# Performance work log

Measured on AMD Instinct MI355X. Metric: run time of the kernel, lower is better.

## Reference

```python
import jax, jax.numpy as jnp
import numpy as np

N, H, OUT, R, E, B = 50000, 64, 64, 50, 800000, 4  # nodes, hidden, out, relations, edges, blocks


def _glorot(k, shape):
    fan_in, fan_out = shape[-2], shape[-1]
    s = (6.0 / (fan_in + fan_out)) ** 0.5
    return jax.random.uniform(k, shape, jnp.float32, -s, s)


def setup_inputs() -> dict:
    key = jax.random.key(0)
    ks = jax.random.split(key, 12)
    db = H // B
    inp = {
        "x": jax.random.normal(ks[0], (N, H), jnp.float32),
        "edge_index": jax.random.randint(ks[1], (2, E), 0, N),
        "edge_type": jax.random.randint(ks[2], (E,), 0, R),
        # hidden RGCNConv layers: block-diagonal relation weights [R,B,db,db]
        "w0_rel": _glorot(ks[3], (R, B, db, db)),
        "w0_root": _glorot(ks[4], (H, H)),
        "b0": jnp.zeros((H,), jnp.float32),
        "w1_rel": _glorot(ks[5], (R, B, db, db)),
        "w1_root": _glorot(ks[6], (H, H)),
        "b1": jnp.zeros((H,), jnp.float32),
        # final RGCNConv: full per-relation weights [R,H,OUT]
        "w2_rel": _glorot(ks[7], (R, H, OUT)),
        "w2_root": _glorot(ks[8], (H, OUT)),
        "b2": jnp.zeros((OUT,), jnp.float32),
    }
    return inp


def _rgcn_layer(x, src, dst, etype, w_rel, w_root, bias):
    """RGCNConv: per-relation mean aggregation of neighbor features, relation-typed
    transform, plus root (self) transform and bias. Instead of gathering a per-edge
    weight (huge), we segment-sum neighbor features per (dst node, relation) and do
    one batched matmul over relations -- same math, far less traffic."""
    n, d = x.shape
    seg = dst * R + etype                                   # combined (node,rel) id
    msgs = x[src]                                           # [E, d] gather
    s = jax.ops.segment_sum(msgs, seg, num_segments=n * R).reshape(n, R, d)
    cnt = jax.ops.segment_sum(jnp.ones((msgs.shape[0],), x.dtype), seg,
                              num_segments=n * R).reshape(n, R, 1)
    s = s / jnp.maximum(cnt, 1.0)                           # mean per relation
    if w_rel.ndim == 4:                                     # block-diagonal decomposition
        nb, db, do = w_rel.shape[1], w_rel.shape[2], w_rel.shape[3]
        agg = jnp.einsum('nrbd,rbde->nbe', s.reshape(n, R, nb, db), w_rel)
        agg = agg.reshape(n, nb * do)
    else:                                                   # full per-relation weight
        agg = jnp.einsum('nrd,rde->ne', s, w_rel)
    return agg + x @ w_root + bias


def reference(x, edge_index, edge_type,
              w0_rel, w0_root, b0,
              w1_rel, w1_root, b1,
              w2_rel, w2_root, b2):
    src, dst = edge_index[0], edge_index[1]
    h = jax.nn.relu(_rgcn_layer(x, src, dst, edge_type, w0_rel, w0_root, b0))
    # dropout: eval mode (identity)
    h = jax.nn.relu(_rgcn_layer(h, src, dst, edge_type, w1_rel, w1_root, b1))
    return _rgcn_layer(h, src, dst, edge_type, w2_rel, w2_root, b2)
```

## Files before the change

### kernel.cpp

```cpp
#include <hip/hip_runtime.h>
#include <cstdint>
#include <cstddef>

#define N_NODES 50000
#define HDIM 64
#define NREL 50
#define NEDGE 800000
#define DCHUNK 196
#define CHUNKSH 11
#define NCHUNK 25
#define NKEYS (NCHUNK * NREL)
#define KCH 5
#define CAP 36864
#define TILE 8192

typedef __attribute__((ext_vector_type(8))) short short8;
typedef __attribute__((ext_vector_type(4))) float f32x4;

static __device__ __forceinline__ unsigned short f2bf(float f) {
  union { float f; unsigned int u; } v; v.f = f;
  unsigned int u = v.u;
  unsigned int r = (u + 0x7FFFu + ((u >> 16) & 1u)) >> 16;
  return (unsigned short)r;
}


__global__ __launch_bounds__(256) void csort_k(const int* __restrict__ ei,
                                               const int* __restrict__ et,
                                               int* __restrict__ ccur,
                                               int2* __restrict__ ce) {
  __shared__ int chist[32];
  __shared__ int cbase[32];
  int tid = threadIdx.x;
  if (tid < 32) chist[tid] = 0;
  __syncthreads();
  int ebase = blockIdx.x * 1280 + tid;
  int src_[5], dr_[5], ch_[5], loc_[5];
#pragma unroll
  for (int i = 0; i < 5; ++i) {
    int e = ebase + i * 256;
    int src = ei[e];
    int dst = ei[NEDGE + e];
    int r = et[e];
    int ch = dst >> CHUNKSH;
    src_[i] = src;
    dr_[i] = (dst << 6) | r;
    ch_[i] = ch;
    loc_[i] = atomicAdd(&chist[ch], 1);
  }
  __syncthreads();
  if (tid < NCHUNK && chist[tid] > 0)
    cbase[tid] = atomicAdd(&ccur[tid], chist[tid]);
  __syncthreads();
#pragma unroll
  for (int i = 0; i < 5; ++i)
    ce[(size_t)ch_[i] * CAP + cbase[ch_[i]] + loc_[i]] = make_int2(src_[i], dr_[i]);
}

__global__ __launch_bounds__(1024) void msplit_k(const int2* __restrict__ ce,
                                                 const int* __restrict__ ccur,
                                                 int* __restrict__ dcur,
                                                 int* __restrict__ kcur,
                                                 int* __restrict__ dkr) {
  __shared__ int dhist[2048], dbase[2048];
  __shared__ int rhist[64], rbase[64];
  int c = blockIdx.y;
  int len = ccur[c];
  int t0 = blockIdx.x * TILE;
  if (t0 >= len) return;
  int tid = threadIdx.x;
  dhist[tid] = 0;
  dhist[tid + 1024] = 0;
  if (tid < 64) rhist[tid] = 0;
  __syncthreads();
  int n = min(TILE, len - t0);
  const int2* seg = ce + (size_t)c * CAP + t0;
  int pk[8], dr_[8];
#pragma unroll
  for (int k = 0; k < 8; ++k) {
    int j = tid + k * 1024;
    if (j < n) {
      int2 v = seg[j];
      dr_[k] = v.y;
      int d11 = (v.y >> 6) & 2047;
      int rel = v.y & 63;
      int dl = atomicAdd(&dhist[d11], 1);
      int rl = atomicAdd(&rhist[rel], 1);
      pk[k] = (dl << 16) | rl;
    } else {
      pk[k] = -1;
    }
  }
  __syncthreads();
  int h0 = dhist[tid];
  if (h0 > 0) dbase[tid] = atomicAdd(&dcur[(c << CHUNKSH) + tid], h0);
  int h1 = dhist[tid + 1024];
  if (h1 > 0) dbase[tid + 1024] = atomicAdd(&dcur[(c << CHUNKSH) + tid + 1024], h1);
  if (tid < NREL) {
    int hr = rhist[tid];
    if (hr > 0) rbase[tid] = atomicAdd(&kcur[c * NREL + tid], hr);
  }
  __syncthreads();
#pragma unroll
  for (int k = 0; k < 8; ++k) {
    if (pk[k] >= 0) {
      int d11 = (dr_[k] >> 6) & 2047;
      int rel = dr_[k] & 63;
      int drank = dbase[d11] + (pk[k] >> 16);
      int krank = rbase[rel] + (pk[k] & 0xFFFF);
      dkr[(size_t)c * CAP + t0 + tid + k * 1024] = (drank << 16) | krank;
    }
  }
}

__global__ __launch_bounds__(256) void kscan_k(const int* __restrict__ kcur,
                                               int* __restrict__ key_off) {
  __shared__ int a[256], bb[256];
  int t = threadIdx.x;
  int base = t * KCH;
  int local[KCH];
  int s = 0;
#pragma unroll
  for (int i = 0; i < KCH; ++i) {
    int k = base + i;
    int v = (k < NKEYS) ? kcur[k] : 0;
    local[i] = s;
    s += v;
  }
  a[t] = s;
  __syncthreads();
  bool flip = false;
  for (int off = 1; off < 256; off <<= 1) {
    int* c = flip ? bb : a;
    int* n = flip ? a : bb;
    int x = c[t];
    if (t >= off) x += c[t - off];
    n[t] = x;
    __syncthreads();
    flip = !flip;
  }
  int incl = (flip ? bb : a)[t];
  int excl = incl - s;
#pragma unroll
  for (int i = 0; i < KCH; ++i) {
    int k = base + i;
    if (k < NKEYS) key_off[k] = excl + local[i];
  }
  if (t == 255) key_off[NKEYS] = incl;
}

__global__ __launch_bounds__(256) void dsA_k(const int* __restrict__ dcnt,
                                             int* __restrict__ psum) {
  __shared__ int red[256];
  int t = threadIdx.x, b = blockIdx.x;
  int idx = b * DCHUNK + t;
  int v = (t < DCHUNK && idx < N_NODES) ? dcnt[idx] : 0;
  red[t] = v;
  __syncthreads();
  for (int s = 128; s > 0; s >>= 1) {
    if (t < s) red[t] += red[t + s];
    __syncthreads();
  }
  if (t == 0) psum[b] = red[0];
}

__global__ __launch_bounds__(256) void dsB_k(const int* __restrict__ psum,
                                             int* __restrict__ psb,
                                             int* __restrict__ dst_off) {
  __shared__ int a[256], bb[256];
  int t = threadIdx.x;
  int v = psum[t];
  a[t] = v;
  __syncthreads();
  bool flip = false;
  for (int off = 1; off < 256; off <<= 1) {
    int* c = flip ? bb : a;
    int* n = flip ? a : bb;
    int x = c[t];
    if (t >= off) x += c[t - off];
    n[t] = x;
    __syncthreads();
    flip = !flip;
  }
  int incl = (flip ? bb : a)[t];
  psb[t] = incl - v;
  if (t == 255) dst_off[N_NODES] = incl;
}

__global__ __launch_bounds__(256) void dsC_k(const int* __restrict__ dcnt,
                                             const int* __restrict__ psb,
                                             int* __restrict__ dst_off) {
  __shared__ int a[256], bb[256];
  int t = threadIdx.x, b = blockIdx.x;
  int idx = b * DCHUNK + t;
  int v = (t < DCHUNK && idx < N_NODES) ? dcnt[idx] : 0;
  a[t] = v;
  __syncthreads();
  bool flip = false;
  for (int off = 1; off < 256; off <<= 1) {
    int* c = flip ? bb : a;
    int* n = flip ? a : bb;
    int x = c[t];
    if (t >= off) x += c[t - off];
    n[t] = x;
    __syncthreads();
    flip = !flip;
  }
  int incl = (flip ? bb : a)[t];
  if (t < DCHUNK && idx < N_NODES) dst_off[idx] = psb[b] + (incl - v);
}

__global__ __launch_bounds__(1024) void place_k(const int2* __restrict__ ce,
                                                const int* __restrict__ ccur,
                                                const int* __restrict__ dkr,
                                                const int* __restrict__ key_off,
                                                const int* __restrict__ dst_off,
                                                int* __restrict__ es,
                                                int* __restrict__ rpr) {
  int c = blockIdx.y;
  int len = ccur[c];
  int t0 = blockIdx.x * TILE;
  if (t0 >= len) return;
  int tid = threadIdx.x;
  int n = min(TILE, len - t0);
  size_t base = (size_t)c * CAP + t0;
#pragma unroll
  for (int k = 0; k < 8; ++k) {
    int j = tid + k * 1024;
    if (j < n) {
      int2 v = ce[base + j];
      int dk = dkr[base + j];
      int dst = v.y >> 6;
      int rel = v.y & 63;
      int key = c * NREL + rel;
      int pos = key_off[key] + (dk & 0xFFFF);
      int dp = dst_off[dst] + (dk >> 16);
      es[pos] = v.x;
      rpr[dp] = (pos << 6) | rel;
    }
  }
}

__global__ __launch_bounds__(256) void coef_k(const int* __restrict__ rpr,
                                              const int* __restrict__ dst_off,
                                              float* __restrict__ coefd) {
  int lane = threadIdx.x & 63;
  int wv = (blockIdx.x * 256 + threadIdx.x) >> 6;
  int half = lane >> 5, l = lane & 31;
  int dst = wv * 2 + half;
  if (dst >= N_NODES) return;
  int lo = dst_off[dst], hi = dst_off[dst + 1];
  for (int j = lo + l; j < hi; j += 32) {
    int r = rpr[j] & 63;
    int c = 0;
    for (int k = lo; k < hi; ++k) c += ((rpr[k] & 63) == r);
    coefd[j] = 1.0f / (float)c;
  }
}

__global__ void prep_k(const float* __restrict__ w0, const float* __restrict__ w1,
                       const float* __restrict__ w2,
                       const float* __restrict__ wr0f, const float* __restrict__ wr1f,
                       const float* __restrict__ wr2f,
                       unsigned short* __restrict__ Wt0, unsigned short* __restrict__ Wt1,
                       unsigned short* __restrict__ Wt2,
                       unsigned short* __restrict__ Wr0, unsigned short* __restrict__ Wr1,
                       unsigned short* __restrict__ Wr2) {
  int idx = blockIdx.x * 256 + threadIdx.x;
  if (idx < NREL * 4096) {
    int r = idx >> 12, rem = idx & 4095, d = rem >> 6, o = rem & 63;
    int tpos = (r << 12) + (o << 6) + d;
    Wt2[tpos] = f2bf(w2[idx]);
    int b = o >> 4;
    float v0 = 0.f, v1 = 0.f;
    if (b == (d >> 4)) {
      int widx = ((r * 4 + b) * 16 + (d & 15)) * 16 + (o & 15);
      v0 = w0[widx];
      v1 = w1[widx];
    }
    Wt0[tpos] = f2bf(v0);
    Wt1[tpos] = f2bf(v1);
  }
  if (idx < 4096) {
    int d = idx >> 6, o = idx & 63;
    int tpos = (o << 6) + d;
    Wr0[tpos] = f2bf(wr0f[idx]);
    Wr1[tpos] = f2bf(wr1f[idx]);
    Wr2[tpos] = f2bf(wr2f[idx]);
  }
}

__global__ void conv_k(const float* __restrict__ in, unsigned short* __restrict__ out) {
  int i = blockIdx.x * 256 + threadIdx.x;
  out[i] = f2bf(in[i]);
}


__global__ __launch_bounds__(256) void root_k(const unsigned short* __restrict__ xbf,
                                              const unsigned short* __restrict__ wr,
                                              const float* __restrict__ bias,
                                              unsigned short* __restrict__ hbf) {
  int wid = threadIdx.x >> 6, lane = threadIdx.x & 63;
  int n15 = lane & 15, quad = lane >> 4;
  int t = blockIdx.x * 4 + wid;
  if (t >= N_NODES / 16) return;
  short8 bfr[4][2];
#pragma unroll
  for (int nb = 0; nb < 4; ++nb)
#pragma unroll
    for (int k = 0; k < 2; ++k)
      bfr[nb][k] = *reinterpret_cast<const short8*>(wr + ((nb * 16 + n15) << 6) + k * 32 + quad * 8);
  float bv[4];
#pragma unroll
  for (int nb = 0; nb < 4; ++nb) bv[nb] = bias[nb * 16 + n15];

  int base = t * 16;
  const short8* xr = reinterpret_cast<const short8*>(xbf + (size_t)(base + n15) * 64);
  short8 a0 = xr[quad], a1 = xr[4 + quad];
  f32x4 acc[4];
#pragma unroll
  for (int nb = 0; nb < 4; ++nb) acc[nb] = (f32x4){0.f, 0.f, 0.f, 0.f};
#pragma unroll
  for (int nb = 0; nb < 4; ++nb) {
    acc[nb] = __builtin_amdgcn_mfma_f32_16x16x32_bf16(a0, bfr[nb][0], acc[nb], 0, 0, 0);
    acc[nb] = __builtin_amdgcn_mfma_f32_16x16x32_bf16(a1, bfr[nb][1], acc[nb], 0, 0, 0);
  }
#pragma unroll
  for (int i = 0; i < 4; ++i) {
    int node = base + quad * 4 + i;
#pragma unroll
    for (int nb = 0; nb < 4; ++nb)
      hbf[(size_t)node * 64 + nb * 16 + n15] = f2bf(acc[nb][i] + bv[nb]);
  }
}

__global__ __launch_bounds__(256) void edge_k(const unsigned short* __restrict__ xbf,
                                              const unsigned short* __restrict__ wt,
                                              const int* __restrict__ es,
                                              const int* __restrict__ key_off,
                                              unsigned short* __restrict__ msg) {
  int key = blockIdx.y;
  int lo = key_off[key], hi = key_off[key + 1];
  if (lo >= hi) return;
  int wid = threadIdx.x >> 6, lane = threadIdx.x & 63;
  int n15 = lane & 15, quad = lane >> 4;
  const unsigned short* wr = wt + ((size_t)(key % NREL) << 12);
  short8 bfr[4][2];
#pragma unroll
  for (int nb = 0; nb < 4; ++nb)
#pragma unroll
    for (int k = 0; k < 2; ++k)
      bfr[nb][k] = *reinterpret_cast<const short8*>(wr + ((nb * 16 + n15) << 6) + k * 32 + quad * 8);

  int ntiles = (hi - lo + 15) >> 4;
  for (int t = blockIdx.x * 4 + wid; t < ntiles; t += gridDim.x * 4) {
    int base = lo + t * 16;
    int eidx = base + n15;
    if (eidx > NEDGE - 1) eidx = NEDGE - 1;
    int src = es[eidx];
    const short8* xr = reinterpret_cast<const short8*>(xbf + (size_t)src * 64);
    short8 a0 = xr[quad], a1 = xr[4 + quad];
    f32x4 acc[4];
#pragma unroll
    for (int nb = 0; nb < 4; ++nb) acc[nb] = (f32x4){0.f, 0.f, 0.f, 0.f};
#pragma unroll
    for (int nb = 0; nb < 4; ++nb) {
      acc[nb] = __builtin_amdgcn_mfma_f32_16x16x32_bf16(a0, bfr[nb][0], acc[nb], 0, 0, 0);
      acc[nb] = __builtin_amdgcn_mfma_f32_16x16x32_bf16(a1, bfr[nb][1], acc[nb], 0, 0, 0);
    }
#pragma unroll
    for (int i = 0; i < 4; ++i) {
      int e2 = base + quad * 4 + i;
      if (e2 < hi) {
        size_t row = (size_t)e2 * 64;
#pragma unroll
        for (int nb = 0; nb < 4; ++nb)
          msg[row + nb * 16 + n15] = f2bf(acc[nb][i]);
      }
    }
  }
}

__global__ __launch_bounds__(256) void agg_k(const unsigned short* __restrict__ hbf,
                                             const unsigned short* __restrict__ msg,
                                             const float* __restrict__ coefd,
                                             const int* __restrict__ rpr,
                                             const int* __restrict__ dst_off,
                                             float* __restrict__ outf,
                                             unsigned short* __restrict__ outbf,
                                             int mode) {
  int lane = threadIdx.x & 63;
  int wv = (blockIdx.x * 256 + threadIdx.x) >> 6;
  int half = lane >> 5, l = lane & 31;
  int dst = wv * 2 + half;
  if (dst >= N_NODES) return;
  int lo = dst_off[dst], hi = dst_off[dst + 1];
  const unsigned int* h32 = reinterpret_cast<const unsigned int*>(hbf);
  unsigned int hu = __builtin_nontemporal_load(h32 + (size_t)dst * 32 + l);
  union { unsigned int u; float f; } hx, hy;
  hx.u = (hu & 0xFFFFu) << 16;
  hy.u = hu & 0xFFFF0000u;
  float ax = hx.f, ay = hy.f;
  const unsigned int* m32 = reinterpret_cast<const unsigned int*>(msg);
  int j = lo;
  for (; j + 4 <= hi; j += 4) {
    int q0 = rpr[j] >> 6, q1 = rpr[j + 1] >> 6, q2 = rpr[j + 2] >> 6, q3 = rpr[j + 3] >> 6;
    float c0 = coefd[j], c1 = coefd[j + 1], c2 = coefd[j + 2], c3 = coefd[j + 3];
    unsigned int u0 = __builtin_nontemporal_load(m32 + q0 * 32 + l);
    unsigned int u1 = __builtin_nontemporal_load(m32 + q1 * 32 + l);
    unsigned int u2 = __builtin_nontemporal_load(m32 + q2 * 32 + l);
    unsigned int u3 = __builtin_nontemporal_load(m32 + q3 * 32 + l);
    union { unsigned int u; float f; } cx, cy;
    cx.u = (u0 & 0xFFFFu) << 16; cy.u = u0 & 0xFFFF0000u; ax += c0 * cx.f; ay += c0 * cy.f;
    cx.u = (u1 & 0xFFFFu) << 16; cy.u = u1 & 0xFFFF0000u; ax += c1 * cx.f; ay += c1 * cy.f;
    cx.u = (u2 & 0xFFFFu) << 16; cy.u = u2 & 0xFFFF0000u; ax += c2 * cx.f; ay += c2 * cy.f;
    cx.u = (u3 & 0xFFFFu) << 16; cy.u = u3 & 0xFFFF0000u; ax += c3 * cx.f; ay += c3 * cy.f;
  }
  for (; j < hi; ++j) {
    float c = coefd[j];
    int pos = rpr[j] >> 6;
    unsigned int u = __builtin_nontemporal_load(m32 + pos * 32 + l);
    union { unsigned int u; float f; } cx, cy;
    cx.u = (u & 0xFFFFu) << 16;
    cy.u = u & 0xFFFF0000u;
    ax += c * cx.f;
    ay += c * cy.f;
  }
  if (mode == 0) {
    float fx = fmaxf(ax, 0.f), fy = fmaxf(ay, 0.f);
    unsigned int pk = ((unsigned int)f2bf(fy) << 16) | (unsigned int)f2bf(fx);
    *reinterpret_cast<unsigned int*>(outbf + (size_t)dst * 64 + 2 * l) = pk;
  } else {
    float2 o2; o2.x = ax; o2.y = ay;
    *reinterpret_cast<float2*>(outf + (size_t)dst * 64 + 2 * l) = o2;
  }
}


extern "C" void kernel_launch(void* const* d_in, const int* in_sizes, int n_in,
                              void* d_out, int out_size, void* d_ws, size_t ws_size,
                              hipStream_t stream) {
  const float* x   = (const float*)d_in[0];
  const int*   ei  = (const int*)d_in[1];
  const int*   et  = (const int*)d_in[2];
  const float* w0  = (const float*)d_in[3];
  const float* wr0 = (const float*)d_in[4];
  const float* b0  = (const float*)d_in[5];
  const float* w1  = (const float*)d_in[6];
  const float* wr1 = (const float*)d_in[7];
  const float* b1  = (const float*)d_in[8];
  const float* w2  = (const float*)d_in[9];
  const float* wr2 = (const float*)d_in[10];
  const float* b2  = (const float*)d_in[11];
  float* out = (float*)d_out;

  char* p = (char*)d_ws;
  auto take = [&](size_t bytes) -> char* {
    char* q = p;
    p += (bytes + 255) & ~(size_t)255;
    return q;
  };
  char*  zbase   = p;
  int*   ccur    = (int*)take(32 * 4);
  int*   dcur    = (int*)take((size_t)NCHUNK * 2048 * 4);
  int*   kcur    = (int*)take((size_t)NKEYS * 4);
  size_t zbytes  = (size_t)(p - zbase);
  int*   key_off = (int*)take((size_t)(NKEYS + 1) * 4);
  int*   dst_off = (int*)take((size_t)(N_NODES + 1) * 4);
  int*   psum    = (int*)take(256 * 4);
  int*   psb     = (int*)take(256 * 4);
  int2*  ce      = (int2*)take((size_t)NCHUNK * CAP * 8);
  int*   dkr     = (int*)take((size_t)NCHUNK * CAP * 4);
  int*   es      = (int*)take((size_t)NEDGE * 4);
  int*   rpr     = (int*)take((size_t)NEDGE * 4);
  float* coefd   = (float*)take((size_t)NEDGE * 4);
  unsigned short* xbf = (unsigned short*)take((size_t)N_NODES * 64 * 2);
  unsigned short* hbf = (unsigned short*)take((size_t)N_NODES * 64 * 2);
  unsigned short* msg = (unsigned short*)take((size_t)NEDGE * 64 * 2);
  unsigned short* Wt0 = (unsigned short*)take((size_t)NREL * 4096 * 2);
  unsigned short* Wt1 = (unsigned short*)take((size_t)NREL * 4096 * 2);
  unsigned short* Wt2 = (unsigned short*)take((size_t)NREL * 4096 * 2);
  unsigned short* Wr0 = (unsigned short*)take(4096 * 2);
  unsigned short* Wr1 = (unsigned short*)take(4096 * 2);
  unsigned short* Wr2 = (unsigned short*)take(4096 * 2);

  hipMemsetAsync(zbase, 0, zbytes, stream);
  csort_k<<<NEDGE / 1280, 256, 0, stream>>>(ei, et, ccur, ce);
  dim3 mg(5, NCHUNK);
  msplit_k<<<mg, 1024, 0, stream>>>(ce, ccur, dcur, kcur, dkr);
  kscan_k<<<1, 256, 0, stream>>>(kcur, key_off);
  dsA_k<<<256, 256, 0, stream>>>(dcur, psum);
  dsB_k<<<1, 256, 0, stream>>>(psum, psb, dst_off);
  dsC_k<<<256, 256, 0, stream>>>(dcur, psb, dst_off);
  place_k<<<mg, 1024, 0, stream>>>(ce, ccur, dkr, key_off, dst_off, es, rpr);
  coef_k<<<N_NODES / 8, 256, 0, stream>>>(rpr, dst_off, coefd);
  prep_k<<<(NREL * 4096 + 255) / 256, 256, 0, stream>>>(w0, w1, w2, wr0, wr1, wr2,
                                                        Wt0, Wt1, Wt2, Wr0, Wr1, Wr2);

  const int conv_blocks = N_NODES * 64 / 256;
  const int root_blocks = (N_NODES / 16 + 3) / 4;
  const int agg_blocks  = N_NODES / 8;
  dim3 eg(2, NKEYS);

  conv_k<<<conv_blocks, 256, 0, stream>>>(x, xbf);
  root_k<<<root_blocks, 256, 0, stream>>>(xbf, Wr0, b0, hbf);
  edge_k<<<eg, 256, 0, stream>>>(xbf, Wt0, es, key_off, msg);
  agg_k<<<agg_blocks, 256, 0, stream>>>(hbf, msg, coefd, rpr, dst_off, nullptr, xbf, 0);
  root_k<<<root_blocks, 256, 0, stream>>>(xbf, Wr1, b1, hbf);
  edge_k<<<eg, 256, 0, stream>>>(xbf, Wt1, es, key_off, msg);
  agg_k<<<agg_blocks, 256, 0, stream>>>(hbf, msg, coefd, rpr, dst_off, nullptr, xbf, 0);
  root_k<<<root_blocks, 256, 0, stream>>>(xbf, Wr2, b2, hbf);
  edge_k<<<eg, 256, 0, stream>>>(xbf, Wt2, es, key_off, msg);
  agg_k<<<agg_blocks, 256, 0, stream>>>(hbf, msg, coefd, rpr, dst_off, out, nullptr, 1);
}
```

Measured before the change: 379.4 us.

## Sub-bucket edges by source range within each relation key for gather locality

The per-(chunk, relation) edge sort key is refined with 32 source-node buckets (src>>11), so edges in each key segment are ordered roughly by source. This should improve cache locality of the x/h row gathers in edge_k. The key-offset scan grows to 40960 entries and becomes a three-kernel scan. edge_k now gives each block a contiguous range of tiles instead of striding across them, so each block's gathers stay in nearby source ranges. The cost is larger shared histograms in msplit_k, more global atomics and two extra small launches.

```diff
diff --git a/kernel.cpp b/kernel.cpp
--- a/kernel.cpp
+++ b/kernel.cpp
@@ -10,7 +10,9 @@
 #define CHUNKSH 11
 #define NCHUNK 25
 #define NKEYS (NCHUNK * NREL)
-#define KCH 5
+#define NKBKT 32
+#define NFINE 1600
+#define NKEY2 40960
 #define CAP 36864
 #define TILE 8192
 
@@ -63,7 +65,7 @@
                                                  int* __restrict__ kcur,
                                                  int* __restrict__ dkr) {
   __shared__ int dhist[2048], dbase[2048];
-  __shared__ int rhist[64], rbase[64];
+  __shared__ int khist[NFINE], kbase[NFINE];
   int c = blockIdx.y;
   int len = ccur[c];
   int t0 = blockIdx.x * TILE;
@@ -71,11 +73,11 @@
   int tid = threadIdx.x;
   dhist[tid] = 0;
   dhist[tid + 1024] = 0;
-  if (tid < 64) rhist[tid] = 0;
+  for (int k = tid; k < NFINE; k += 1024) khist[k] = 0;
   __syncthreads();
   int n = min(TILE, len - t0);
   const int2* seg = ce + (size_t)c * CAP + t0;
-  int pk[8], dr_[8];
+  int pk[8], dr_[8], kk_[8];
 #pragma unroll
   for (int k = 0; k < 8; ++k) {
     int j = tid + k * 1024;
@@ -84,9 +86,11 @@
       dr_[k] = v.y;
       int d11 = (v.y >> 6) & 2047;
       int rel = v.y & 63;
+      int kk = rel * NKBKT + (v.x >> 11);
+      kk_[k] = kk;
       int dl = atomicAdd(&dhist[d11], 1);
-      int rl = atomicAdd(&rhist[rel], 1);
-      pk[k] = (dl << 16) | rl;
+      int kl = atomicAdd(&khist[kk], 1);
+      pk[k] = (dl << 16) | kl;
     } else {
       pk[k] = -1;
     }
@@ -96,38 +100,42 @@
   if (h0 > 0) dbase[tid] = atomicAdd(&dcur[(c << CHUNKSH) + tid], h0);
   int h1 = dhist[tid + 1024];
   if (h1 > 0) dbase[tid + 1024] = atomicAdd(&dcur[(c << CHUNKSH) + tid + 1024], h1);
-  if (tid < NREL) {
-    int hr = rhist[tid];
-    if (hr > 0) rbase[tid] = atomicAdd(&kcur[c * NREL + tid], hr);
+  for (int k2 = tid; k2 < NFINE; k2 += 1024) {
+    int hk = khist[k2];
+    if (hk > 0) kbase[k2] = atomicAdd(&kcur[c * NFINE + k2], hk);
   }
   __syncthreads();
 #pragma unroll
   for (int k = 0; k < 8; ++k) {
     if (pk[k] >= 0) {
       int d11 = (dr_[k] >> 6) & 2047;
-      int rel = dr_[k] & 63;
       int drank = dbase[d11] + (pk[k] >> 16);
-      int krank = rbase[rel] + (pk[k] & 0xFFFF);
+      int krank = kbase[kk_[k]] + (pk[k] & 0xFFFF);
       dkr[(size_t)c * CAP + t0 + tid + k * 1024] = (drank << 16) | krank;
     }
   }
 }
 
-__global__ __launch_bounds__(256) void kscan_k(const int* __restrict__ kcur,
-                                               int* __restrict__ key_off) {
+
+__global__ __launch_bounds__(256) void ksA_k(const int* __restrict__ kcur,
+                                             int* __restrict__ kps) {
+  __shared__ int red[256];
+  int t = threadIdx.x, b = blockIdx.x;
+  red[t] = kcur[b * 256 + t];
+  __syncthreads();
+  for (int s = 128; s > 0; s >>= 1) {
+    if (t < s) red[t] += red[t + s];
+    __syncthreads();
+  }
+  if (t == 0) kps[b] = red[0];
+}
+
+__global__ __launch_bounds__(256) void ksB_k(const int* __restrict__ kps,
+                                             int* __restrict__ kpsb) {
   __shared__ int a[256], bb[256];
   int t = threadIdx.x;
-  int base = t * KCH;
-  int local[KCH];
-  int s = 0;
-#pragma unroll
-  for (int i = 0; i < KCH; ++i) {
-    int k = base + i;
-    int v = (k < NKEYS) ? kcur[k] : 0;
-    local[i] = s;
-    s += v;
-  }
-  a[t] = s;
+  int v = (t < NKEY2 / 256) ? kps[t] : 0;
+  a[t] = v;
   __syncthreads();
   bool flip = false;
   for (int off = 1; off < 256; off <<= 1) {
@@ -140,13 +148,29 @@
     flip = !flip;
   }
   int incl = (flip ? bb : a)[t];
-  int excl = incl - s;
-#pragma unroll
-  for (int i = 0; i < KCH; ++i) {
-    int k = base + i;
-    if (k < NKEYS) key_off[k] = excl + local[i];
-  }
-  if (t == 255) key_off[NKEYS] = incl;
+  kpsb[t] = incl - v;
+}
+
+__global__ __launch_bounds__(256) void ksC_k(const int* __restrict__ kcur,
+                                             const int* __restrict__ kpsb,
+                                             int* __restrict__ key_off) {
+  __shared__ int a[256], bb[256];
+  int t = threadIdx.x, b = blockIdx.x;
+  int v = kcur[b * 256 + t];
+  a[t] = v;
+  __syncthreads();
+  bool flip = false;
+  for (int off = 1; off < 256; off <<= 1) {
+    int* c = flip ? bb : a;
+    int* n = flip ? a : bb;
+    int x = c[t];
+    if (t >= off) x += c[t - off];
+    n[t] = x;
+    __syncthreads();
+    flip = !flip;
+  }
+  int incl = (flip ? bb : a)[t];
+  key_off[b * 256 + t] = kpsb[b] + (incl - v);
 }
 
 __global__ __launch_bounds__(256) void dsA_k(const int* __restrict__ dcnt,
@@ -232,8 +256,8 @@
       int dk = dkr[base + j];
       int dst = v.y >> 6;
       int rel = v.y & 63;
-      int key = c * NREL + rel;
-      int pos = key_off[key] + (dk & 0xFFFF);
+      int kk = rel * NKBKT + (v.x >> 11);
+      int pos = key_off[c * NFINE + kk] + (dk & 0xFFFF);
       int dp = dst_off[dst] + (dk >> 16);
       es[pos] = v.x;
       rpr[dp] = (pos << 6) | rel;
@@ -339,12 +363,12 @@
                                               const int* __restrict__ es,
                                               const int* __restrict__ key_off,
                                               unsigned short* __restrict__ msg) {
-  int key = blockIdx.y;
-  int lo = key_off[key], hi = key_off[key + 1];
+  int ck = blockIdx.y;
+  int lo = key_off[ck * NKBKT], hi = key_off[ck * NKBKT + NKBKT];
   if (lo >= hi) return;
   int wid = threadIdx.x >> 6, lane = threadIdx.x & 63;
   int n15 = lane & 15, quad = lane >> 4;
-  const unsigned short* wr = wt + ((size_t)(key % NREL) << 12);
+  const unsigned short* wr = wt + ((size_t)(ck % NREL) << 12);
   short8 bfr[4][2];
 #pragma unroll
   for (int nb = 0; nb < 4; ++nb)
@@ -353,7 +377,10 @@
       bfr[nb][k] = *reinterpret_cast<const short8*>(wr + ((nb * 16 + n15) << 6) + k * 32 + quad * 8);
 
   int ntiles = (hi - lo + 15) >> 4;
-  for (int t = blockIdx.x * 4 + wid; t < ntiles; t += gridDim.x * 4) {
+  int per = (ntiles + gridDim.x - 1) / gridDim.x;
+  int tb0 = blockIdx.x * per;
+  int tb1 = min(ntiles, tb0 + per);
+  for (int t = tb0 + wid; t < tb1; t += 4) {
     int base = lo + t * 16;
     int eidx = base + n15;
     if (eidx > NEDGE - 1) eidx = NEDGE - 1;
@@ -463,12 +490,14 @@
   char*  zbase   = p;
   int*   ccur    = (int*)take(32 * 4);
   int*   dcur    = (int*)take((size_t)NCHUNK * 2048 * 4);
-  int*   kcur    = (int*)take((size_t)NKEYS * 4);
+  int*   kcur    = (int*)take((size_t)NKEY2 * 4);
   size_t zbytes  = (size_t)(p - zbase);
-  int*   key_off = (int*)take((size_t)(NKEYS + 1) * 4);
+  int*   key_off = (int*)take((size_t)NKEY2 * 4);
   int*   dst_off = (int*)take((size_t)(N_NODES + 1) * 4);
   int*   psum    = (int*)take(256 * 4);
   int*   psb     = (int*)take(256 * 4);
+  int*   kps     = (int*)take(256 * 4);
+  int*   kpsb    = (int*)take(256 * 4);
   int2*  ce      = (int2*)take((size_t)NCHUNK * CAP * 8);
   int*   dkr     = (int*)take((size_t)NCHUNK * CAP * 4);
   int*   es      = (int*)take((size_t)NEDGE * 4);
@@ -488,7 +517,9 @@
   csort_k<<<NEDGE / 1280, 256, 0, stream>>>(ei, et, ccur, ce);
   dim3 mg(5, NCHUNK);
   msplit_k<<<mg, 1024, 0, stream>>>(ce, ccur, dcur, kcur, dkr);
-  kscan_k<<<1, 256, 0, stream>>>(kcur, key_off);
+  ksA_k<<<NKEY2 / 256, 256, 0, stream>>>(kcur, kps);
+  ksB_k<<<1, 256, 0, stream>>>(kps, kpsb);
+  ksC_k<<<NKEY2 / 256, 256, 0, stream>>>(kcur, kpsb, key_off);
   dsA_k<<<256, 256, 0, stream>>>(dcur, psum);
   dsB_k<<<1, 256, 0, stream>>>(psum, psb, dst_off);
   dsC_k<<<256, 256, 0, stream>>>(dcur, psb, dst_off);
```

Result: no change. 385.2 us (+1.5%).
